# Kernel tuning notes

Hardware: AMD Instinct MI355X
Metric: run time of the kernel (lower is better)

## Reference

```python
import jax, jax.numpy as jnp
import numpy as np

E = 100000          # number of edges
IN_FEATS = 256      # in_edge_feats
HIDDEN = 128        # hidden_size
K = 16              # neighbors per edge (uniform-degree rendering of ragged lists)


def setup_inputs() -> dict:
    key = jax.random.key(0)
    k1, k2, k3, k4 = jax.random.split(key, 4)
    edge_feats = jax.random.normal(k1, (E, IN_FEATS), dtype=jnp.float32)
    neighbors = jax.random.randint(k2, (E, K), 0, E, dtype=jnp.int32)
    # Linear params (torch Linear: y = x @ W^T + b; here W stored as [in, out])
    W = jax.random.normal(k3, (IN_FEATS, HIDDEN), dtype=jnp.float32) / np.sqrt(IN_FEATS)
    b = jax.random.normal(k4, (HIDDEN,), dtype=jnp.float32) * 0.01
    return {"edge_feats": edge_feats, "neighbors": neighbors, "W": W, "b": b}


def reference(edge_feats, neighbors, W, b):
    # Dense linear transform of all edge features: [E, H]
    t = edge_feats @ W + b
    # Gather each edge's K neighbor transformed features and sum: [E, K, H] -> [E, H]
    nbr_sum = jnp.take(t, neighbors, axis=0).sum(axis=1)
    # agg[i] = t[i] + sum_{n in neighbors[i]} t[n]
    return t + nbr_sum
```

## Files before the change

### kernel.cpp

```cpp
#include <hip/hip_runtime.h>
#include <hip/hip_bf16.h>
#include <stdint.h>

#define E_EDGES 100000
#define IN_F    256
#define HID     128
#define KNB     16
#define NCHUNK  ((E_EDGES + 63) / 64)
#define GEMM_GRID 512

#define NS          16
#define SLICE_ROWS  6250
#define GCHUNKS     5
#define EDGES_PER_BLK (GCHUNKS * 16)
#define GATHER_GRID (E_EDGES / EDGES_PER_BLK)

typedef short bf16x8 __attribute__((ext_vector_type(8)));
typedef float f32x4  __attribute__((ext_vector_type(4)));

__device__ __forceinline__ unsigned short f2bf(float f) {
    union { float f; unsigned u; } v; v.f = f;
    unsigned u = v.u;
    u += 0x7fffu + ((u >> 16) & 1u);
    return (unsigned short)(u >> 16);
}

__global__ void conv_w_kernel(const float* __restrict__ W, unsigned short* __restrict__ Wtf) {
    int d = blockIdx.x * 256 + threadIdx.x;
    int f = d >> 6, L = d & 63;
    int k0 = f >> 3, ct = f & 7, quad = L >> 4, l15 = L & 15;
    int n  = ct * 16 + l15;
    int kb = (k0 * 4 + quad) * 8;
    const float* wp = W + (size_t)kb * HID + n;
    unsigned short h[8];
    #pragma unroll
    for (int j = 0; j < 8; ++j) h[j] = f2bf(wp[(size_t)j * HID]);
    uint4 o;
    o.x = (unsigned)h[0] | ((unsigned)h[1] << 16);
    o.y = (unsigned)h[2] | ((unsigned)h[3] << 16);
    o.z = (unsigned)h[4] | ((unsigned)h[5] << 16);
    o.w = (unsigned)h[6] | ((unsigned)h[7] << 16);
    *(uint4*)(Wtf + (size_t)d * 8) = o;
}

__launch_bounds__(256, 2)
__global__ void gemm_t_kernel(const float* __restrict__ A,
                              const unsigned short* __restrict__ Wtf,
                              const float* __restrict__ bias,
                              unsigned short* __restrict__ T) {
    __shared__ unsigned short Bs[32768];
    const int tid  = threadIdx.x;
    const int wave = tid >> 6;
    const int lane = tid & 63;
    const int l15  = lane & 15;
    const int quad = lane >> 4;

    int c = blockIdx.x;
    int arow = c * 64 + wave * 16 + l15;
    if (arow >= E_EDGES) arow = E_EDGES - 1;
    const float* ap = A + (size_t)arow * IN_F + quad * 8;
    float4 af32[16];
    #pragma unroll
    for (int k0 = 0; k0 < 8; ++k0) {
        af32[2 * k0]     = *(const float4*)(ap + k0 * 32);
        af32[2 * k0 + 1] = *(const float4*)(ap + k0 * 32 + 4);
    }

    #pragma unroll
    for (int it = 0; it < 16; ++it) {
        int d = it * 256 + tid;
        *(uint4*)(Bs + (size_t)d * 8) = *(const uint4*)(Wtf + (size_t)d * 8);
    }

    float4 bv4[8];
    #pragma unroll
    for (int ct = 0; ct < 8; ++ct)
        bv4[ct] = *(const float4*)(bias + ct * 16 + quad * 4);

    __syncthreads();

    for (; c < NCHUNK; c += GEMM_GRID) {
        bf16x8 apre[8];
        #pragma unroll
        for (int k0 = 0; k0 < 8; ++k0) {
            float4 lo = af32[2 * k0], hi = af32[2 * k0 + 1];
            bf16x8 f;
            f[0] = (short)f2bf(lo.x); f[1] = (short)f2bf(lo.y);
            f[2] = (short)f2bf(lo.z); f[3] = (short)f2bf(lo.w);
            f[4] = (short)f2bf(hi.x); f[5] = (short)f2bf(hi.y);
            f[6] = (short)f2bf(hi.z); f[7] = (short)f2bf(hi.w);
            apre[k0] = f;
        }

        {
            int cn = c + GEMM_GRID;
            int arow2 = cn * 64 + wave * 16 + l15;
            if (arow2 >= E_EDGES) arow2 = E_EDGES - 1;
            const float* ap2 = A + (size_t)arow2 * IN_F + quad * 8;
            #pragma unroll
            for (int k0 = 0; k0 < 8; ++k0) {
                af32[2 * k0]     = *(const float4*)(ap2 + k0 * 32);
                af32[2 * k0 + 1] = *(const float4*)(ap2 + k0 * 32 + 4);
            }
        }
        __builtin_amdgcn_sched_barrier(0);

        f32x4 acc[8] = {};
        #pragma unroll
        for (int k0 = 0; k0 < 8; ++k0) {
            #pragma unroll
            for (int ct = 0; ct < 8; ++ct) {
                bf16x8 bf = *(const bf16x8*)(Bs + ((size_t)((k0 * 8 + ct) * 64 + lane)) * 8);
                acc[ct] = __builtin_amdgcn_mfma_f32_16x16x32_bf16(bf, apre[k0], acc[ct], 0, 0, 0);
            }
        }

        const int row = c * 64 + wave * 16 + l15;
        if (row < E_EDGES) {
            unsigned short* tp = T + (size_t)row * HID + quad * 4;
            #pragma unroll
            for (int ct = 0; ct < 8; ++ct) {
                unsigned short h0 = f2bf(acc[ct][0] + bv4[ct].x);
                unsigned short h1 = f2bf(acc[ct][1] + bv4[ct].y);
                unsigned short h2 = f2bf(acc[ct][2] + bv4[ct].z);
                unsigned short h3 = f2bf(acc[ct][3] + bv4[ct].w);
                uint2 o;
                o.x = (unsigned)h0 | ((unsigned)h1 << 16);
                o.y = (unsigned)h2 | ((unsigned)h3 << 16);
                *(uint2*)(tp + ct * 16) = o;
            }
        }
    }
}

__device__ __forceinline__ float u2f(unsigned u) {
    union { unsigned u; float f; } c; c.u = u; return c.f;
}
__device__ __forceinline__ f32x4 declo(uint4 v) {
    f32x4 r = { u2f(v.x << 16), u2f(v.x & 0xffff0000u),
                u2f(v.y << 16), u2f(v.y & 0xffff0000u) };
    return r;
}
__device__ __forceinline__ f32x4 dechi(uint4 v) {
    f32x4 r = { u2f(v.z << 16), u2f(v.z & 0xffff0000u),
                u2f(v.w << 16), u2f(v.w & 0xffff0000u) };
    return r;
}

__launch_bounds__(256, 5)
__global__ void gather_sum_kernel(const unsigned short* __restrict__ T,
                                  const int* __restrict__ nbr,
                                  float* __restrict__ out) {
    __shared__ int ssort[EDGES_PER_BLK * 17];
    __shared__ int soff[EDGES_PER_BLK * 17];
    __shared__ int scur[EDGES_PER_BLK * 17];

    const int tid   = threadIdx.x;
    const int edge0 = blockIdx.x * EDGES_PER_BLK;
    const int el    = tid >> 4;
    const int lane  = tid & 15;

    if (tid < EDGES_PER_BLK) {
        const int t = tid;
        const unsigned self = (unsigned)(edge0 + t);
        const int* np = nbr + (size_t)(edge0 + t) * KNB;

        unsigned idxs[KNB];
        #pragma unroll
        for (int k = 0; k < KNB; k += 4) {
            uint4 q = *(const uint4*)(np + k);
            idxs[k] = q.x; idxs[k + 1] = q.y; idxs[k + 2] = q.z; idxs[k + 3] = q.w;
        }

        #pragma unroll
        for (int s = 0; s < NS; ++s) scur[t * 17 + s] = 0;
        #pragma unroll
        for (int k = 0; k < KNB; ++k)
            scur[t * 17 + idxs[k] / SLICE_ROWS] += 1;
        scur[t * 17 + self / SLICE_ROWS] += 1;

        int run = 0;
        #pragma unroll
        for (int s = 0; s < NS; ++s) {
            int c0 = scur[t * 17 + s];
            soff[t * 17 + s] = run;
            scur[t * 17 + s] = run;
            run += c0;
        }
        soff[t * 17 + NS] = run;

        #pragma unroll
        for (int k = 0; k < KNB; ++k) {
            int s = (int)(idxs[k] / SLICE_ROWS);
            ssort[t * 17 + scur[t * 17 + s]++] = (int)idxs[k];
        }
        {
            int s = (int)(self / SLICE_ROWS);
            ssort[t * 17 + scur[t * 17 + s]++] = (int)self;
        }
    }
    __syncthreads();

    const unsigned short* Tb = T + (size_t)lane * 8;

#define DECL_CHUNK(c) \
    f32x4 accL##c = {0.f, 0.f, 0.f, 0.f}; \
    f32x4 accH##c = {0.f, 0.f, 0.f, 0.f}; \
    int   cur##c  = 0; \
    const int base##c = (c * 16 + el) * 17;

    DECL_CHUNK(0) DECL_CHUNK(1) DECL_CHUNK(2) DECL_CHUNK(3) DECL_CHUNK(4)
#undef DECL_CHUNK

#define RUN_CHUNK(c) { \
    const int e_ = soff[base##c + s + 1]; \
    int j_ = cur##c; \
    cur##c = e_; \
    if (j_ < e_) { \
        int idx_ = ssort[base##c + j_]; \
        uint4 v_ = *(const uint4*)(Tb + (size_t)idx_ * HID); \
        for (++j_; j_ < e_; ++j_) { \
            int idx2_ = ssort[base##c + j_]; \
            uint4 v2_ = *(const uint4*)(Tb + (size_t)idx2_ * HID); \
            accL##c += declo(v_); \
            accH##c += dechi(v_); \
            v_ = v2_; \
        } \
        accL##c += declo(v_); \
        accH##c += dechi(v_); \
    } }

    for (int s = 0; s < NS; ++s) {
        RUN_CHUNK(0)
        RUN_CHUNK(1)
        RUN_CHUNK(2)
        RUN_CHUNK(3)
        RUN_CHUNK(4)
    }
#undef RUN_CHUNK

#define STORE_CHUNK(c) { \
    const int edge_ = edge0 + c * 16 + el; \
    float* op_ = out + (size_t)edge_ * HID + lane * 8; \
    __builtin_nontemporal_store(accL##c, (f32x4*)op_); \
    __builtin_nontemporal_store(accH##c, (f32x4*)(op_ + 4)); \
    }

    STORE_CHUNK(0) STORE_CHUNK(1) STORE_CHUNK(2) STORE_CHUNK(3) STORE_CHUNK(4)
#undef STORE_CHUNK
}

extern "C" void kernel_launch(void* const* d_in, const int* in_sizes, int n_in,
                              void* d_out, int out_size, void* d_ws, size_t ws_size,
                              hipStream_t stream) {
    const float* edge_feats = (const float*)d_in[0];
    const int*   neighbors  = (const int*)d_in[1];
    const float* W          = (const float*)d_in[2];
    const float* b          = (const float*)d_in[3];
    float*       out        = (float*)d_out;

    unsigned short* Wtf = (unsigned short*)d_ws;
    unsigned short* T   = (unsigned short*)d_ws + (size_t)IN_F * HID;

    conv_w_kernel<<<16, 256, 0, stream>>>(W, Wtf);
    gemm_t_kernel<<<GEMM_GRID, 256, 0, stream>>>(edge_feats, Wtf, b, T);
    gather_sum_kernel<<<GATHER_GRID, 256, 0, stream>>>(T, neighbors, out);
}
```

Before: 248.0 us.

## Gather five neighbor chunks in lockstep with predicated loads and coarser slices

```diff
diff --git a/kernel.cpp b/kernel.cpp
--- a/kernel.cpp
+++ b/kernel.cpp
@@ -9,8 +9,8 @@
 #define NCHUNK  ((E_EDGES + 63) / 64)
 #define GEMM_GRID 512
 
-#define NS          16
-#define SLICE_ROWS  6250
+#define NS          8
+#define SLICE_ROWS  12500
 #define GCHUNKS     5
 #define EDGES_PER_BLK (GCHUNKS * 16)
 #define GATHER_GRID (E_EDGES / EDGES_PER_BLK)
@@ -147,13 +147,13 @@
     return r;
 }
 
-__launch_bounds__(256, 5)
+__launch_bounds__(256, 4)
 __global__ void gather_sum_kernel(const unsigned short* __restrict__ T,
                                   const int* __restrict__ nbr,
                                   float* __restrict__ out) {
     __shared__ int ssort[EDGES_PER_BLK * 17];
-    __shared__ int soff[EDGES_PER_BLK * 17];
-    __shared__ int scur[EDGES_PER_BLK * 17];
+    __shared__ int soff[EDGES_PER_BLK * 9];
+    __shared__ int scur[EDGES_PER_BLK * 9];
 
     const int tid   = threadIdx.x;
     const int edge0 = blockIdx.x * EDGES_PER_BLK;
@@ -173,30 +173,30 @@
         }
 
         #pragma unroll
-        for (int s = 0; s < NS; ++s) scur[t * 17 + s] = 0;
+        for (int s = 0; s < NS; ++s) scur[t * 9 + s] = 0;
         #pragma unroll
         for (int k = 0; k < KNB; ++k)
-            scur[t * 17 + idxs[k] / SLICE_ROWS] += 1;
-        scur[t * 17 + self / SLICE_ROWS] += 1;
+            scur[t * 9 + idxs[k] / SLICE_ROWS] += 1;
+        scur[t * 9 + self / SLICE_ROWS] += 1;
 
         int run = 0;
         #pragma unroll
         for (int s = 0; s < NS; ++s) {
-            int c0 = scur[t * 17 + s];
-            soff[t * 17 + s] = run;
-            scur[t * 17 + s] = run;
+            int c0 = scur[t * 9 + s];
+            soff[t * 9 + s] = run;
+            scur[t * 9 + s] = run;
             run += c0;
         }
-        soff[t * 17 + NS] = run;
+        soff[t * 9 + NS] = run;
 
         #pragma unroll
         for (int k = 0; k < KNB; ++k) {
             int s = (int)(idxs[k] / SLICE_ROWS);
-            ssort[t * 17 + scur[t * 17 + s]++] = (int)idxs[k];
+            ssort[t * 17 + scur[t * 9 + s]++] = (int)idxs[k];
         }
         {
             int s = (int)(self / SLICE_ROWS);
-            ssort[t * 17 + scur[t * 17 + s]++] = (int)self;
+            ssort[t * 17 + scur[t * 9 + s]++] = (int)self;
         }
     }
     __syncthreads();
@@ -206,38 +206,52 @@
 #define DECL_CHUNK(c) \
     f32x4 accL##c = {0.f, 0.f, 0.f, 0.f}; \
     f32x4 accH##c = {0.f, 0.f, 0.f, 0.f}; \
-    int   cur##c  = 0; \
-    const int base##c = (c * 16 + el) * 17;
+    int   j##c = 0; \
+    const int sb##c = (c * 16 + el) * 17; \
+    const int ob##c = (c * 16 + el) * 9;
 
     DECL_CHUNK(0) DECL_CHUNK(1) DECL_CHUNK(2) DECL_CHUNK(3) DECL_CHUNK(4)
 #undef DECL_CHUNK
 
-#define RUN_CHUNK(c) { \
-    const int e_ = soff[base##c + s + 1]; \
-    int j_ = cur##c; \
-    cur##c = e_; \
-    if (j_ < e_) { \
-        int idx_ = ssort[base##c + j_]; \
-        uint4 v_ = *(const uint4*)(Tb + (size_t)idx_ * HID); \
-        for (++j_; j_ < e_; ++j_) { \
-            int idx2_ = ssort[base##c + j_]; \
-            uint4 v2_ = *(const uint4*)(Tb + (size_t)idx2_ * HID); \
-            accL##c += declo(v_); \
-            accH##c += dechi(v_); \
-            v_ = v2_; \
-        } \
-        accL##c += declo(v_); \
-        accH##c += dechi(v_); \
-    } }
-
     for (int s = 0; s < NS; ++s) {
-        RUN_CHUNK(0)
-        RUN_CHUNK(1)
-        RUN_CHUNK(2)
-        RUN_CHUNK(3)
-        RUN_CHUNK(4)
-    }
-#undef RUN_CHUNK
+        const int e0 = soff[ob0 + s + 1];
+        const int e1 = soff[ob1 + s + 1];
+        const int e2 = soff[ob2 + s + 1];
+        const int e3 = soff[ob3 + s + 1];
+        const int e4 = soff[ob4 + s + 1];
+
+        while (true) {
+            const bool p0 = j0 < e0, p1 = j1 < e1, p2 = j2 < e2,
+                       p3 = j3 < e3, p4 = j4 < e4;
+            if (!__any((int)(p0 | p1 | p2 | p3 | p4))) break;
+
+            const int i0 = ssort[sb0 + (p0 ? j0 : 16)];
+            const int i1 = ssort[sb1 + (p1 ? j1 : 16)];
+            const int i2 = ssort[sb2 + (p2 ? j2 : 16)];
+            const int i3 = ssort[sb3 + (p3 ? j3 : 16)];
+            const int i4 = ssort[sb4 + (p4 ? j4 : 16)];
+
+            const uint4 v0 = *(const uint4*)(Tb + (size_t)i0 * HID);
+            const uint4 v1 = *(const uint4*)(Tb + (size_t)i1 * HID);
+            const uint4 v2 = *(const uint4*)(Tb + (size_t)i2 * HID);
+            const uint4 v3 = *(const uint4*)(Tb + (size_t)i3 * HID);
+            const uint4 v4 = *(const uint4*)(Tb + (size_t)i4 * HID);
+            __builtin_amdgcn_sched_barrier(0);
+
+#define ACC_CHUNK(c) { \
+            uint4 w_; \
+            w_.x = p##c ? v##c.x : 0u; \
+            w_.y = p##c ? v##c.y : 0u; \
+            w_.z = p##c ? v##c.z : 0u; \
+            w_.w = p##c ? v##c.w : 0u; \
+            accL##c += declo(w_); \
+            accH##c += dechi(w_); \
+            j##c += (int)p##c; }
+
+            ACC_CHUNK(0) ACC_CHUNK(1) ACC_CHUNK(2) ACC_CHUNK(3) ACC_CHUNK(4)
+#undef ACC_CHUNK
+        }
+    }
 
 #define STORE_CHUNK(c) { \
     const int edge_ = edge0 + c * 16 + el; \
```

Result: no change. 243.7 us (-1.7%).
